# Performance work log

Measured on AMD Instinct MI355X. Metric: run time of the kernel, lower is better.

## Reference

```python
import jax, jax.numpy as jnp
from jax import lax
import numpy as np

H = 256      # encoder_hidden
F = 256      # variance predictor filter_size
K = 3        # kernel_size
NBINS = 256  # variance_embedding n_bins
B, S, T = 64, 512, 2048


def conv1d(x, w, b, pad):
    # x: [B, L, Cin], w: [K, Cin, Cout] -> [B, L, Cout]
    y = lax.conv_general_dilated(x, w, window_strides=(1,), padding=[(pad, pad)],
                                 dimension_numbers=('NWC', 'WIO', 'NWC'))
    return y + b


def layer_norm(x, g, b, eps=1e-5):
    mu = jnp.mean(x, -1, keepdims=True)
    v = jnp.mean((x - mu) ** 2, -1, keepdims=True)
    return (x - mu) * lax.rsqrt(v + eps) * g + b


def predictor(x, mask, w1, b1, g1, be1, w2, b2, g2, be2, lw, lb):
    h = jax.nn.relu(conv1d(x, w1, b1, (K - 1) // 2))
    h = layer_norm(h, g1, be1)
    h = jax.nn.relu(conv1d(h, w2, b2, 1))  # padding=1 hardcoded in original conv1d_2
    h = layer_norm(h, g2, be2)
    out = (h @ lw + lb)[..., 0]            # [B, L]
    return jnp.where(mask, 0.0, out)       # masked_fill(mask, 0.0)


def setup_inputs():
    key = jax.random.key(0)
    ks = jax.random.split(key, 16)
    inp = {
        'x': jax.random.normal(ks[0], (B, S, H), jnp.float32),
        'pitch_target': jax.random.normal(ks[1], (B, S), jnp.float32),
        'energy_target': jax.random.normal(ks[2], (B, S), jnp.float32),
        'src_mask': jnp.zeros((B, S), bool),
        'duration': jax.random.randint(ks[3], (B, S), 0, 4, jnp.int32),
        'max_len': T,
    }
    i = 4
    for p in ['d', 'p', 'e']:
        inp[p + '_w1'] = jax.random.normal(ks[i], (K, H, F), jnp.float32) * 0.05; i += 1
        inp[p + '_b1'] = jnp.zeros((F,), jnp.float32)
        inp[p + '_g1'] = jnp.ones((F,), jnp.float32)
        inp[p + '_be1'] = jnp.zeros((F,), jnp.float32)
        inp[p + '_w2'] = jax.random.normal(ks[i], (K, F, F), jnp.float32) * 0.05; i += 1
        inp[p + '_b2'] = jnp.zeros((F,), jnp.float32)
        inp[p + '_g2'] = jnp.ones((F,), jnp.float32)
        inp[p + '_be2'] = jnp.zeros((F,), jnp.float32)
        inp[p + '_lw'] = jax.random.normal(ks[i], (F, 1), jnp.float32) * 0.05; i += 1
        inp[p + '_lb'] = jnp.zeros((1,), jnp.float32)
    inp['p_table'] = jax.random.normal(ks[i], (NBINS, H), jnp.float32) * 0.02; i += 1
    inp['e_table'] = jax.random.normal(ks[i], (NBINS, H), jnp.float32) * 0.02
    return inp


def reference(x, pitch_target, energy_target, src_mask, duration, max_len,
              d_w1, d_b1, d_g1, d_be1, d_w2, d_b2, d_g2, d_be2, d_lw, d_lb,
              p_w1, p_b1, p_g1, p_be1, p_w2, p_b2, p_g2, p_be2, p_lw, p_lb,
              e_w1, e_b1, e_g1, e_be1, e_w2, e_b2, e_g2, e_be2, e_lw, e_lb,
              p_table, e_table):
    # linear-quantized bins over the data range (stats.json min/max -> [-2, 2] for randn data)
    bins = jnp.linspace(-2.0, 2.0, NBINS - 1, dtype=jnp.float32)

    log_d_pred = predictor(x, src_mask, d_w1, d_b1, d_g1, d_be1, d_w2, d_b2, d_g2, d_be2, d_lw, d_lb)

    # phoneme-level pitch (training path: target given -> embed bucketized target)
    p_pred = predictor(x, src_mask, p_w1, p_b1, p_g1, p_be1, p_w2, p_b2, p_g2, p_be2, p_lw, p_lb)
    p_emb = p_table[jnp.searchsorted(bins, pitch_target, side='left')]  # torch.bucketize(right=False)
    x = x + p_emb

    # phoneme-level energy (predictor runs on x AFTER pitch embedding, as in original)
    e_pred = predictor(x, src_mask, e_w1, e_b1, e_g1, e_be1, e_w2, e_b2, e_g2, e_be2, e_lw, e_lb)
    e_emb = e_table[jnp.searchsorted(bins, energy_target, side='left')]
    x = x + e_emb

    # Length regulation: expand phoneme i duration[b, i] times, pad to max_len.
    cum = jnp.cumsum(duration, axis=1)                 # [B, S]
    mel_len = cum[:, -1]                               # [B]
    frames = jnp.arange(max_len)                       # [T]
    # frame t maps to first phoneme i with cum[i] > t
    idx = jax.vmap(lambda c: jnp.searchsorted(c, frames, side='right'))(cum)  # [B, T]
    idx = jnp.minimum(idx, duration.shape[1] - 1)
    mel = jnp.take_along_axis(x, idx[:, :, None], axis=1)                     # [B, T, H]
    valid = frames[None, :] < mel_len[:, None]
    mel = jnp.where(valid[:, :, None], mel, 0.0)       # zero-pad beyond mel_len

    d_rounded = duration
    return (mel, p_pred, e_pred, log_d_pred, d_rounded, mel_len)
```

## Files before the change

kernel.cpp:

```cpp
#include <hip/hip_runtime.h>
#include <cstdint>
#include <cstddef>


#define HH 256
#define SS 512
#define BB 64
#define TT 2048
#define LSTR 264

typedef __bf16 bf16;
typedef __attribute__((ext_vector_type(8))) __bf16 bf16x8;
typedef __attribute__((ext_vector_type(4))) __bf16 bf16x4;
typedef __attribute__((ext_vector_type(4))) float f32x4;

static constexpr size_t WSZ = (size_t)3 * HH * HH;

__device__ __forceinline__ float edge_val(int j) {
    const float step = 4.0f / 254.0f;
    if (j == 254) return 2.0f;
    return __fadd_rn(-2.0f, __fmul_rn((float)j, step));
}
__device__ __forceinline__ int bucket256(float v) {
    int lo = 0, hi = 255;
    while (lo < hi) {
        int mid = (lo + hi) >> 1;
        if (edge_val(mid) < v) lo = mid + 1; else hi = mid;
    }
    return lo;
}

__global__ __launch_bounds__(256) void prep_kernel(
    const float* __restrict__ w0, const float* __restrict__ w1,
    const float* __restrict__ w2, const float* __restrict__ w3,
    const float* __restrict__ w4, const float* __restrict__ w5,
    bf16* __restrict__ wp,
    const int* __restrict__ dur, int* __restrict__ idxb, int* __restrict__ mli,
    float* __restrict__ drnd, float* __restrict__ mlen)
{
    const int tid = threadIdx.x;
    if (blockIdx.x < 18) {
        const int cv = blockIdx.x / 3, k = blockIdx.x % 3;
        const float* wsel[6] = {w0, w1, w2, w3, w4, w5};
        const float* wk = wsel[cv] + (size_t)k * HH * HH;
        bf16* o = wp + ((size_t)(cv * 3 + k)) * HH * HH;
        for (int fb = 0; fb < 16; ++fb) {
            #pragma unroll
            for (int h = 0; h < 2; ++h) {
                const int idx  = tid + 256 * h;
                const int kcb  = idx >> 6, lane = idx & 63;
                const int f    = fb * 16 + (lane & 15);
                const int c0   = kcb * 32 + (lane >> 4) * 8;
                bf16x8 v;
                #pragma unroll
                for (int j = 0; j < 8; ++j) v[j] = (bf16)wk[(size_t)(c0 + j) * HH + f];
                *(bf16x8*)(o + (((size_t)fb * 8 + kcb) * 64 + lane) * 8) = v;
            }
        }
    } else {
        __shared__ int sb[SS];
        const int b = blockIdx.x - 18;
        const int d0 = dur[b * SS + tid];
        const int d1 = dur[b * SS + tid + 256];
        drnd[b * SS + tid]       = (float)d0;
        drnd[b * SS + tid + 256] = (float)d1;
        sb[tid]       = d0;
        sb[tid + 256] = d1;
        __syncthreads();
        for (int off = 1; off < SS; off <<= 1) {
            const int a0 = (tid >= off) ? sb[tid - off] : 0;
            const int a1 = (tid + 256 >= off) ? sb[tid + 256 - off] : 0;
            __syncthreads();
            sb[tid] += a0;
            sb[tid + 256] += a1;
            __syncthreads();
        }
        {
            const int hi = sb[tid], lo = hi - d0;
            for (int j = lo; j < hi; ++j) idxb[b * TT + j] = tid;
        }
        {
            const int hi = sb[tid + 256], lo = hi - d1;
            for (int j = lo; j < hi; ++j) idxb[b * TT + j] = tid + 256;
        }
        if (tid == 255) { mlen[b] = (float)sb[SS - 1]; mli[b] = sb[SS - 1]; }
    }
}

struct Args3 {
    const float* bias[3];
    const float* g[3];
    const float* be[3];
    const float* lw[3];
    const float* lb[3];
    float*       out[3];
};

__global__ __launch_bounds__(256, 3) void conv_fused(
    const float* __restrict__ x,
    const float* __restrict__ pt,
    const float* __restrict__ ptab,
    const bf16* __restrict__ wpk,
    Args3 a1, Args3 a2,
    const uint8_t* __restrict__ mask)
{
    __shared__ alignas(16) bf16 tile[82 * LSTR];
    __shared__ float red_s[80][4], red_q[80][4];
    __shared__ float ln_m[80], ln_r[80];
    __shared__ int remb[82];

    const int tid    = threadIdx.x;
    const int pred   = blockIdx.x >> 9;
    const int within = blockIdx.x & 511;
    const int b      = within >> 3;
    const int s0     = (within & 7) * 64;
    const bool emb   = (pred == 2);

    const int lane = tid & 63;
    const int wv   = tid >> 6;

    const float* xb  = x + (size_t)b * SS * HH;
    const bf16* wt1 = wpk + (size_t)(pred * 2) * WSZ;
    const bf16* wt2 = wt1 + WSZ;

    if (emb) {
        if (tid < 82) {
            const int s = s0 - 9 + tid;
            remb[tid] = (s >= 0 && s < SS) ? bucket256(pt[b * SS + s]) : 0;
        }
        __syncthreads();
    }

    for (int idx = tid; idx < 82 * 64; idx += 256) {
        const int r  = idx >> 6, c4 = (idx & 63) << 2;
        const int s  = s0 - 9 + r;
        float4 v = make_float4(0.f, 0.f, 0.f, 0.f);
        if (s >= 0 && s < SS) {
            v = *(const float4*)(xb + (size_t)s * HH + c4);
            if (emb) {
                const float4 tv = *(const float4*)(ptab + (size_t)remb[r] * HH + c4);
                v.x += tv.x; v.y += tv.y; v.z += tv.z; v.w += tv.w;
            }
        }
        bf16x4 bv = {(bf16)v.x, (bf16)v.y, (bf16)v.z, (bf16)v.w};
        *(bf16x4*)&tile[r * LSTR + c4] = bv;
    }
    __syncthreads();

    const int ln15 = lane & 15;
    const int g8   = (lane >> 4) << 3;
    const int q4   = (lane >> 4) << 2;

    f32x4 bini[4];
    #pragma unroll
    for (int mf = 0; mf < 4; ++mf)
        #pragma unroll
        for (int i = 0; i < 4; ++i)
            bini[mf][i] = a1.bias[pred][64 * wv + 16 * mf + q4 + i];

    f32x4 acc1[4][5];
    #pragma unroll
    for (int mf = 0; mf < 4; ++mf)
        #pragma unroll
        for (int sf = 0; sf < 5; ++sf) acc1[mf][sf] = bini[mf];

    #pragma unroll 2
    for (int t = 0; t < 24; ++t) {
        const int k = t >> 3, kcb = t & 7;
        const int kc = kcb << 5;
        bf16x8 aw[4], bx[5];
        const bf16* bp = wt1 + ((((size_t)k * 16 + wv * 4) * 8 + kcb) << 9)
                       + (size_t)lane * 8;
        #pragma unroll
        for (int mf = 0; mf < 4; ++mf)
            aw[mf] = *(const bf16x8*)(bp + ((size_t)mf << 12));
        #pragma unroll
        for (int sf = 0; sf < 5; ++sf)
            bx[sf] = *(const bf16x8*)&tile[(16 * sf + ln15 + k) * LSTR + kc + g8];
        __builtin_amdgcn_s_setprio(1);
        #pragma unroll
        for (int mf = 0; mf < 4; ++mf)
            #pragma unroll
            for (int sf = 0; sf < 5; ++sf)
                acc1[mf][sf] = __builtin_amdgcn_mfma_f32_16x16x32_bf16(
                    aw[mf], bx[sf], acc1[mf][sf], 0, 0, 0);
        __builtin_amdgcn_s_setprio(0);
    }

    bf16x8 aw20[4];
    {
        const bf16* bp2 = wt2 + (((size_t)wv * 4) * 8 << 9) + (size_t)lane * 8;
        #pragma unroll
        for (int mf = 0; mf < 4; ++mf)
            aw20[mf] = *(const bf16x8*)(bp2 + ((size_t)mf << 12));
    }

    #pragma unroll
    for (int mf = 0; mf < 4; ++mf)
        #pragma unroll
        for (int sf = 0; sf < 5; ++sf)
            #pragma unroll
            for (int i = 0; i < 4; ++i)
                acc1[mf][sf][i] = fmaxf(acc1[mf][sf][i], 0.f);

    #pragma unroll
    for (int sf = 0; sf < 5; ++sf) {
        float s = 0.f, q = 0.f;
        #pragma unroll
        for (int mf = 0; mf < 4; ++mf)
            #pragma unroll
            for (int i = 0; i < 4; ++i) {
                const float v = acc1[mf][sf][i];
                s += v; q += v * v;
            }
        s += __shfl_xor(s, 16); s += __shfl_xor(s, 32);
        q += __shfl_xor(q, 16); q += __shfl_xor(q, 32);
        if (lane < 16) { red_s[16 * sf + lane][wv] = s; red_q[16 * sf + lane][wv] = q; }
    }
    __syncthreads();
    if (tid < 80) {
        const float s = red_s[tid][0] + red_s[tid][1] + red_s[tid][2] + red_s[tid][3];
        const float q = red_q[tid][0] + red_q[tid][1] + red_q[tid][2] + red_q[tid][3];
        const float mean = s * (1.f / 256.f);
        const float var  = q * (1.f / 256.f) - mean * mean;
        ln_m[tid] = mean;
        ln_r[tid] = rsqrtf(var + 1e-5f);
    }
    __syncthreads();

    {
        float g1v[4][4], be1v[4][4];
        #pragma unroll
        for (int mf = 0; mf < 4; ++mf)
            #pragma unroll
            for (int i = 0; i < 4; ++i) {
                const int f1 = 64 * wv + 16 * mf + q4 + i;
                g1v[mf][i]  = a1.g[pred][f1];
                be1v[mf][i] = a1.be[pred][f1];
            }
        #pragma unroll
        for (int sf = 0; sf < 5; ++sf) {
            const int o  = 16 * sf + ln15;
            const int hr = o - 7;
            const float mean = ln_m[o], rs = ln_r[o];
            const bool ok = (o >= 7 && o <= 72);
            #pragma unroll
            for (int mf = 0; mf < 4; ++mf) {
                bf16x4 hv;
                #pragma unroll
                for (int i = 0; i < 4; ++i)
                    hv[i] = (bf16)((acc1[mf][sf][i] - mean) * rs * g1v[mf][i] + be1v[mf][i]);
                if (ok)
                    *(bf16x4*)&tile[hr * LSTR + 64 * wv + 16 * mf + q4] = hv;
            }
        }
    }
    __syncthreads();
    if (tid < 64) {
        if (s0 == 0)       *(uint2*)&tile[tid * 4]            = make_uint2(0u, 0u);
        if (s0 == SS - 64) *(uint2*)&tile[65 * LSTR + tid * 4] = make_uint2(0u, 0u);
    }
    __syncthreads();

    #pragma unroll
    for (int mf = 0; mf < 4; ++mf)
        #pragma unroll
        for (int i = 0; i < 4; ++i)
            bini[mf][i] = a2.bias[pred][64 * wv + 16 * mf + q4 + i];

    f32x4 acc2[4][4];
    #pragma unroll
    for (int mf = 0; mf < 4; ++mf)
        #pragma unroll
        for (int sf = 0; sf < 4; ++sf) acc2[mf][sf] = bini[mf];

#define S2_STEP(AW_, K_, KCB_) do {                                            \
    const int kc_ = (KCB_) << 5;                                               \
    bf16x8 bx_[4];                                                             \
    _Pragma("unroll")                                                          \
    for (int sf_ = 0; sf_ < 4; ++sf_)                                          \
        bx_[sf_] = *(const bf16x8*)&tile[(16 * sf_ + ln15 + (K_)) * LSTR       \
                                         + kc_ + g8];                          \
    __builtin_amdgcn_s_setprio(1);                                             \
    _Pragma("unroll")                                                          \
    for (int mf_ = 0; mf_ < 4; ++mf_)                                          \
        _Pragma("unroll")                                                      \
        for (int sf_ = 0; sf_ < 4; ++sf_)                                      \
            acc2[mf_][sf_] = __builtin_amdgcn_mfma_f32_16x16x32_bf16(          \
                AW_[mf_], bx_[sf_], acc2[mf_][sf_], 0, 0, 0);                  \
    __builtin_amdgcn_s_setprio(0);                                             \
} while (0)

    S2_STEP(aw20, 0, 0);
    #pragma unroll 2
    for (int t = 1; t < 24; ++t) {
        const int k = t >> 3, kcb = t & 7;
        bf16x8 aw[4];
        const bf16* bp = wt2 + ((((size_t)k * 16 + wv * 4) * 8 + kcb) << 9)
                       + (size_t)lane * 8;
        #pragma unroll
        for (int mf = 0; mf < 4; ++mf)
            aw[mf] = *(const bf16x8*)(bp + ((size_t)mf << 12));
        S2_STEP(aw, k, kcb);
    }
#undef S2_STEP

    #pragma unroll
    for (int mf = 0; mf < 4; ++mf)
        #pragma unroll
        for (int sf = 0; sf < 4; ++sf)
            #pragma unroll
            for (int i = 0; i < 4; ++i)
                acc2[mf][sf][i] = fmaxf(acc2[mf][sf][i], 0.f);

    #pragma unroll
    for (int sf = 0; sf < 4; ++sf) {
        float s = 0.f, q = 0.f;
        #pragma unroll
        for (int mf = 0; mf < 4; ++mf)
            #pragma unroll
            for (int i = 0; i < 4; ++i) {
                const float v = acc2[mf][sf][i];
                s += v; q += v * v;
            }
        s += __shfl_xor(s, 16); s += __shfl_xor(s, 32);
        q += __shfl_xor(q, 16); q += __shfl_xor(q, 32);
        if (lane < 16) { red_s[16 * sf + lane][wv] = s; red_q[16 * sf + lane][wv] = q; }
    }
    __syncthreads();
    if (tid < 64) {
        const float s = red_s[tid][0] + red_s[tid][1] + red_s[tid][2] + red_s[tid][3];
        const float q = red_q[tid][0] + red_q[tid][1] + red_q[tid][2] + red_q[tid][3];
        const float mean = s * (1.f / 256.f);
        const float var  = q * (1.f / 256.f) - mean * mean;
        ln_m[tid] = mean;
        ln_r[tid] = rsqrtf(var + 1e-5f);
    }
    __syncthreads();

    {
        float c1v[4][4], cbv[4][4];
        #pragma unroll
        for (int mf = 0; mf < 4; ++mf)
            #pragma unroll
            for (int i = 0; i < 4; ++i) {
                const int f2 = 64 * wv + 16 * mf + q4 + i;
                const float lwv = a2.lw[pred][f2];
                c1v[mf][i] = a2.g[pred][f2] * lwv;
                cbv[mf][i] = a2.be[pred][f2] * lwv;
            }
        #pragma unroll
        for (int sf = 0; sf < 4; ++sf) {
            const int so = 16 * sf + ln15;
            const float mean = ln_m[so], rs = ln_r[so];
            float t = 0.f;
            #pragma unroll
            for (int mf = 0; mf < 4; ++mf)
                #pragma unroll
                for (int i = 0; i < 4; ++i)
                    t += (acc2[mf][sf][i] - mean) * rs * c1v[mf][i] + cbv[mf][i];
            t += __shfl_xor(t, 16); t += __shfl_xor(t, 32);
            if (lane < 16) red_s[16 * sf + lane][wv] = t;
        }
        __syncthreads();
        if (tid < 64) {
            const int gr = b * SS + s0 + tid;
            const float dv = red_s[tid][0] + red_s[tid][1] + red_s[tid][2] + red_s[tid][3]
                           + a2.lb[pred][0];
            a2.out[pred][gr] = mask[gr] ? 0.f : dv;
        }
    }
}

__global__ __launch_bounds__(256) void gather_kernel(
    const float* __restrict__ x,
    const float* __restrict__ ptab, const float* __restrict__ pt,
    const float* __restrict__ etab, const float* __restrict__ et,
    const int* __restrict__ idxb, const int* __restrict__ mli,
    float* __restrict__ mel)
{
    const int lane = threadIdx.x & 63;
    for (int row = blockIdx.x * 4 + (threadIdx.x >> 6); row < BB * TT; row += 4096 * 4) {
        const int b = row >> 11;
        const int t = row & (TT - 1);
        float4 v = make_float4(0.f, 0.f, 0.f, 0.f);
        if (t < mli[b]) {
            const int idx = idxb[row];
            const size_t src = ((size_t)b * SS + idx) * HH + lane * 4;
            v = *(const float4*)(x + src);
            const int pb = bucket256(pt[b * SS + idx]);
            const int eb = bucket256(et[b * SS + idx]);
            const float4 pv = *(const float4*)(ptab + (size_t)pb * HH + lane * 4);
            const float4 ev = *(const float4*)(etab + (size_t)eb * HH + lane * 4);
            v.x += pv.x + ev.x; v.y += pv.y + ev.y; v.z += pv.z + ev.z; v.w += pv.w + ev.w;
        }
        *(float4*)(mel + (size_t)row * HH + lane * 4) = v;
    }
}

extern "C" void kernel_launch(void* const* d_in, const int* in_sizes, int n_in,
                              void* d_out, int out_size, void* d_ws, size_t ws_size,
                              hipStream_t stream) {
    (void)in_sizes; (void)n_in; (void)out_size; (void)ws_size;

    const float*   x      = (const float*)d_in[0];
    const float*   pitch  = (const float*)d_in[1];
    const float*   energy = (const float*)d_in[2];
    const uint8_t* mask   = (const uint8_t*)d_in[3];
    const int*     dur    = (const int*)d_in[4];
    const float*   ptab   = (const float*)d_in[36];
    const float*   etab   = (const float*)d_in[37];

    float* out = (float*)d_out;
    const size_t N_MEL = (size_t)BB * TT * HH;
    float* out_p  = out + N_MEL;
    float* out_e  = out_p + (size_t)BB * SS;
    float* out_ld = out_e + (size_t)BB * SS;
    float* out_dr = out_ld + (size_t)BB * SS;
    float* out_ml = out_dr + (size_t)BB * SS;

    bf16* wpk  = (bf16*)d_ws;
    int*  idxb = (int*)(wpk + 6 * WSZ);
    int*  mli  = idxb + (size_t)BB * TT;

    prep_kernel<<<18 + 64, 256, 0, stream>>>(
        (const float*)d_in[6],  (const float*)d_in[10],
        (const float*)d_in[16], (const float*)d_in[20],
        (const float*)d_in[26], (const float*)d_in[30],
        wpk,
        dur, idxb, mli, out_dr, out_ml);

    Args3 a1 = {
        {(const float*)d_in[7],  (const float*)d_in[17], (const float*)d_in[27]},
        {(const float*)d_in[8],  (const float*)d_in[18], (const float*)d_in[28]},
        {(const float*)d_in[9],  (const float*)d_in[19], (const float*)d_in[29]},
        {nullptr, nullptr, nullptr}, {nullptr, nullptr, nullptr},
        {nullptr, nullptr, nullptr}
    };
    Args3 a2 = {
        {(const float*)d_in[11], (const float*)d_in[21], (const float*)d_in[31]},
        {(const float*)d_in[12], (const float*)d_in[22], (const float*)d_in[32]},
        {(const float*)d_in[13], (const float*)d_in[23], (const float*)d_in[33]},
        {(const float*)d_in[14], (const float*)d_in[24], (const float*)d_in[34]},
        {(const float*)d_in[15], (const float*)d_in[25], (const float*)d_in[35]},
        {out_ld, out_p, out_e}
    };

    conv_fused<<<3 * 512, 256, 0, stream>>>(x, pitch, ptab, wpk, a1, a2, mask);

    gather_kernel<<<4096, 256, 0, stream>>>(x, ptab, pitch, etab, energy, idxb, mli, out);
}
```

Before: 132.4 us.

## Run all three predictors in one block reusing a shared x tile

Instead of launching one block per (predictor, sequence tile), each block now loads the x tile once into shared memory and loops over the three predictors. The pitch embedding is added in place to the bf16 tile before the energy predictor. The conv1 output goes to a separate htile, which also holds the reduction scratch. This cuts the number of x loads and conversions by three, but leaves only 512 blocks with lower occupancy (launch bounds 2), so each block's serial work triples and latency is less well hidden. The embedding add also rounds to bf16 once more than the old fp32 add did.

```diff
diff --git a/kernel.cpp b/kernel.cpp
--- a/kernel.cpp
+++ b/kernel.cpp
@@ -96,7 +96,7 @@
     float*       out[3];
 };
 
-__global__ __launch_bounds__(256, 3) void conv_fused(
+__global__ __launch_bounds__(256, 2) void conv_all3(
     const float* __restrict__ x,
     const float* __restrict__ pt,
     const float* __restrict__ ptab,
@@ -104,46 +104,31 @@
     Args3 a1, Args3 a2,
     const uint8_t* __restrict__ mask)
 {
-    __shared__ alignas(16) bf16 tile[82 * LSTR];
-    __shared__ float red_s[80][4], red_q[80][4];
+    __shared__ alignas(16) bf16 xtile[82 * LSTR];
+    __shared__ alignas(16) bf16 htile[66 * LSTR];
     __shared__ float ln_m[80], ln_r[80];
     __shared__ int remb[82];
-
-    const int tid    = threadIdx.x;
-    const int pred   = blockIdx.x >> 9;
-    const int within = blockIdx.x & 511;
-    const int b      = within >> 3;
-    const int s0     = (within & 7) * 64;
-    const bool emb   = (pred == 2);
-
+    float* red = (float*)htile;
+
+    const int tid  = threadIdx.x;
+    const int b    = blockIdx.x >> 3;
+    const int s0   = (blockIdx.x & 7) * 64;
     const int lane = tid & 63;
     const int wv   = tid >> 6;
 
-    const float* xb  = x + (size_t)b * SS * HH;
-    const bf16* wt1 = wpk + (size_t)(pred * 2) * WSZ;
-    const bf16* wt2 = wt1 + WSZ;
-
-    if (emb) {
-        if (tid < 82) {
-            const int s = s0 - 9 + tid;
-            remb[tid] = (s >= 0 && s < SS) ? bucket256(pt[b * SS + s]) : 0;
-        }
-        __syncthreads();
-    }
-
+    const float* xb = x + (size_t)b * SS * HH;
+
+    if (tid < 82) {
+        const int s = s0 - 9 + tid;
+        remb[tid] = (s >= 0 && s < SS) ? bucket256(pt[b * SS + s]) : 0;
+    }
     for (int idx = tid; idx < 82 * 64; idx += 256) {
-        const int r  = idx >> 6, c4 = (idx & 63) << 2;
-        const int s  = s0 - 9 + r;
+        const int r = idx >> 6, c4 = (idx & 63) << 2;
+        const int s = s0 - 9 + r;
         float4 v = make_float4(0.f, 0.f, 0.f, 0.f);
-        if (s >= 0 && s < SS) {
-            v = *(const float4*)(xb + (size_t)s * HH + c4);
-            if (emb) {
-                const float4 tv = *(const float4*)(ptab + (size_t)remb[r] * HH + c4);
-                v.x += tv.x; v.y += tv.y; v.z += tv.z; v.w += tv.w;
-            }
-        }
+        if (s >= 0 && s < SS) v = *(const float4*)(xb + (size_t)s * HH + c4);
         bf16x4 bv = {(bf16)v.x, (bf16)v.y, (bf16)v.z, (bf16)v.w};
-        *(bf16x4*)&tile[r * LSTR + c4] = bv;
+        *(bf16x4*)&xtile[r * LSTR + c4] = bv;
     }
     __syncthreads();
 
@@ -151,136 +136,159 @@
     const int g8   = (lane >> 4) << 3;
     const int q4   = (lane >> 4) << 2;
 
-    f32x4 bini[4];
-    #pragma unroll
-    for (int mf = 0; mf < 4; ++mf)
-        #pragma unroll
-        for (int i = 0; i < 4; ++i)
-            bini[mf][i] = a1.bias[pred][64 * wv + 16 * mf + q4 + i];
-
-    f32x4 acc1[4][5];
-    #pragma unroll
-    for (int mf = 0; mf < 4; ++mf)
-        #pragma unroll
-        for (int sf = 0; sf < 5; ++sf) acc1[mf][sf] = bini[mf];
-
-    #pragma unroll 2
-    for (int t = 0; t < 24; ++t) {
-        const int k = t >> 3, kcb = t & 7;
-        const int kc = kcb << 5;
-        bf16x8 aw[4], bx[5];
-        const bf16* bp = wt1 + ((((size_t)k * 16 + wv * 4) * 8 + kcb) << 9)
-                       + (size_t)lane * 8;
-        #pragma unroll
-        for (int mf = 0; mf < 4; ++mf)
-            aw[mf] = *(const bf16x8*)(bp + ((size_t)mf << 12));
-        #pragma unroll
-        for (int sf = 0; sf < 5; ++sf)
-            bx[sf] = *(const bf16x8*)&tile[(16 * sf + ln15 + k) * LSTR + kc + g8];
-        __builtin_amdgcn_s_setprio(1);
-        #pragma unroll
-        for (int mf = 0; mf < 4; ++mf)
+    #pragma unroll 1
+    for (int pred = 0; pred < 3; ++pred) {
+        if (pred == 2) {
+            for (int idx = tid; idx < 82 * 64; idx += 256) {
+                const int r = idx >> 6, c4 = (idx & 63) << 2;
+                bf16x4 v = *(bf16x4*)&xtile[r * LSTR + c4];
+                const float4 tv = *(const float4*)(ptab + (size_t)remb[r] * HH + c4);
+                v[0] = (bf16)((float)v[0] + tv.x);
+                v[1] = (bf16)((float)v[1] + tv.y);
+                v[2] = (bf16)((float)v[2] + tv.z);
+                v[3] = (bf16)((float)v[3] + tv.w);
+                *(bf16x4*)&xtile[r * LSTR + c4] = v;
+            }
+            __syncthreads();
+        }
+
+        const bf16* wt1 = wpk + (size_t)(pred * 2) * WSZ;
+        const bf16* wt2 = wt1 + WSZ;
+
+        f32x4 bini[4];
+        #pragma unroll
+        for (int mf = 0; mf < 4; ++mf)
+            #pragma unroll
+            for (int i = 0; i < 4; ++i)
+                bini[mf][i] = a1.bias[pred][64 * wv + 16 * mf + q4 + i];
+
+        f32x4 acc1[4][5];
+        #pragma unroll
+        for (int mf = 0; mf < 4; ++mf)
+            #pragma unroll
+            for (int sf = 0; sf < 5; ++sf) acc1[mf][sf] = bini[mf];
+
+        #pragma unroll 2
+        for (int t = 0; t < 24; ++t) {
+            const int k = t >> 3, kcb = t & 7;
+            const int kc = kcb << 5;
+            bf16x8 aw[4], bx[5];
+            const bf16* bp = wt1 + ((((size_t)k * 16 + wv * 4) * 8 + kcb) << 9)
+                           + (size_t)lane * 8;
+            #pragma unroll
+            for (int mf = 0; mf < 4; ++mf)
+                aw[mf] = *(const bf16x8*)(bp + ((size_t)mf << 12));
             #pragma unroll
             for (int sf = 0; sf < 5; ++sf)
-                acc1[mf][sf] = __builtin_amdgcn_mfma_f32_16x16x32_bf16(
-                    aw[mf], bx[sf], acc1[mf][sf], 0, 0, 0);
-        __builtin_amdgcn_s_setprio(0);
-    }
-
-    bf16x8 aw20[4];
-    {
-        const bf16* bp2 = wt2 + (((size_t)wv * 4) * 8 << 9) + (size_t)lane * 8;
-        #pragma unroll
-        for (int mf = 0; mf < 4; ++mf)
-            aw20[mf] = *(const bf16x8*)(bp2 + ((size_t)mf << 12));
-    }
-
-    #pragma unroll
-    for (int mf = 0; mf < 4; ++mf)
-        #pragma unroll
-        for (int sf = 0; sf < 5; ++sf)
+                bx[sf] = *(const bf16x8*)&xtile[(16 * sf + ln15 + k) * LSTR + kc + g8];
+            __builtin_amdgcn_s_setprio(1);
+            #pragma unroll
+            for (int mf = 0; mf < 4; ++mf)
+                #pragma unroll
+                for (int sf = 0; sf < 5; ++sf)
+                    acc1[mf][sf] = __builtin_amdgcn_mfma_f32_16x16x32_bf16(
+                        aw[mf], bx[sf], acc1[mf][sf], 0, 0, 0);
+            __builtin_amdgcn_s_setprio(0);
+        }
+
+        bf16x8 aw20[4];
+        {
+            const bf16* bp2 = wt2 + (((size_t)wv * 4) * 8 << 9) + (size_t)lane * 8;
+            #pragma unroll
+            for (int mf = 0; mf < 4; ++mf)
+                aw20[mf] = *(const bf16x8*)(bp2 + ((size_t)mf << 12));
+        }
+
+        #pragma unroll
+        for (int mf = 0; mf < 4; ++mf)
+            #pragma unroll
+            for (int sf = 0; sf < 5; ++sf)
+                #pragma unroll
+                for (int i = 0; i < 4; ++i)
+                    acc1[mf][sf][i] = fmaxf(acc1[mf][sf][i], 0.f);
+
+        #pragma unroll
+        for (int sf = 0; sf < 5; ++sf) {
+            float s = 0.f, q = 0.f;
+            #pragma unroll
+            for (int mf = 0; mf < 4; ++mf)
+                #pragma unroll
+                for (int i = 0; i < 4; ++i) {
+                    const float v = acc1[mf][sf][i];
+                    s += v; q += v * v;
+                }
+            s += __shfl_xor(s, 16); s += __shfl_xor(s, 32);
+            q += __shfl_xor(q, 16); q += __shfl_xor(q, 32);
+            if (lane < 16) {
+                red[(16 * sf + lane) * 4 + wv] = s;
+                red[320 + (16 * sf + lane) * 4 + wv] = q;
+            }
+        }
+        __syncthreads();
+        if (tid < 80) {
+            const float s = red[tid * 4] + red[tid * 4 + 1] + red[tid * 4 + 2] + red[tid * 4 + 3];
+            const float q = red[320 + tid * 4] + red[320 + tid * 4 + 1]
+                          + red[320 + tid * 4 + 2] + red[320 + tid * 4 + 3];
+            const float mean = s * (1.f / 256.f);
+            const float var  = q * (1.f / 256.f) - mean * mean;
+            ln_m[tid] = mean;
+            ln_r[tid] = rsqrtf(var + 1e-5f);
+        }
+        __syncthreads();
+
+        {
+            float g1v[4][4], be1v[4][4];
+            #pragma unroll
+            for (int mf = 0; mf < 4; ++mf)
+                #pragma unroll
+                for (int i = 0; i < 4; ++i) {
+                    const int f1 = 64 * wv + 16 * mf + q4 + i;
+                    g1v[mf][i]  = a1.g[pred][f1];
+                    be1v[mf][i] = a1.be[pred][f1];
+                }
+            #pragma unroll
+            for (int sf = 0; sf < 5; ++sf) {
+                const int o  = 16 * sf + ln15;
+                const int hr = o - 7;
+                const float mean = ln_m[o], rs = ln_r[o];
+                const bool ok = (o >= 7 && o <= 72);
+                #pragma unroll
+                for (int mf = 0; mf < 4; ++mf) {
+                    bf16x4 hv;
+                    #pragma unroll
+                    for (int i = 0; i < 4; ++i)
+                        hv[i] = (bf16)((acc1[mf][sf][i] - mean) * rs * g1v[mf][i] + be1v[mf][i]);
+                    if (ok)
+                        *(bf16x4*)&htile[hr * LSTR + 64 * wv + 16 * mf + q4] = hv;
+                }
+            }
+        }
+        __syncthreads();
+        if (tid < 64) {
+            if (s0 == 0)       *(uint2*)&htile[tid * 4]            = make_uint2(0u, 0u);
+            if (s0 == SS - 64) *(uint2*)&htile[65 * LSTR + tid * 4] = make_uint2(0u, 0u);
+        }
+        __syncthreads();
+
+        #pragma unroll
+        for (int mf = 0; mf < 4; ++mf)
             #pragma unroll
             for (int i = 0; i < 4; ++i)
-                acc1[mf][sf][i] = fmaxf(acc1[mf][sf][i], 0.f);
-
-    #pragma unroll
-    for (int sf = 0; sf < 5; ++sf) {
-        float s = 0.f, q = 0.f;
-        #pragma unroll
-        for (int mf = 0; mf < 4; ++mf)
-            #pragma unroll
-            for (int i = 0; i < 4; ++i) {
-                const float v = acc1[mf][sf][i];
-                s += v; q += v * v;
-            }
-        s += __shfl_xor(s, 16); s += __shfl_xor(s, 32);
-        q += __shfl_xor(q, 16); q += __shfl_xor(q, 32);
-        if (lane < 16) { red_s[16 * sf + lane][wv] = s; red_q[16 * sf + lane][wv] = q; }
-    }
-    __syncthreads();
-    if (tid < 80) {
-        const float s = red_s[tid][0] + red_s[tid][1] + red_s[tid][2] + red_s[tid][3];
-        const float q = red_q[tid][0] + red_q[tid][1] + red_q[tid][2] + red_q[tid][3];
-        const float mean = s * (1.f / 256.f);
-        const float var  = q * (1.f / 256.f) - mean * mean;
-        ln_m[tid] = mean;
-        ln_r[tid] = rsqrtf(var + 1e-5f);
-    }
-    __syncthreads();
-
-    {
-        float g1v[4][4], be1v[4][4];
-        #pragma unroll
-        for (int mf = 0; mf < 4; ++mf)
-            #pragma unroll
-            for (int i = 0; i < 4; ++i) {
-                const int f1 = 64 * wv + 16 * mf + q4 + i;
-                g1v[mf][i]  = a1.g[pred][f1];
-                be1v[mf][i] = a1.be[pred][f1];
-            }
-        #pragma unroll
-        for (int sf = 0; sf < 5; ++sf) {
-            const int o  = 16 * sf + ln15;
-            const int hr = o - 7;
-            const float mean = ln_m[o], rs = ln_r[o];
-            const bool ok = (o >= 7 && o <= 72);
-            #pragma unroll
-            for (int mf = 0; mf < 4; ++mf) {
-                bf16x4 hv;
-                #pragma unroll
-                for (int i = 0; i < 4; ++i)
-                    hv[i] = (bf16)((acc1[mf][sf][i] - mean) * rs * g1v[mf][i] + be1v[mf][i]);
-                if (ok)
-                    *(bf16x4*)&tile[hr * LSTR + 64 * wv + 16 * mf + q4] = hv;
-            }
-        }
-    }
-    __syncthreads();
-    if (tid < 64) {
-        if (s0 == 0)       *(uint2*)&tile[tid * 4]            = make_uint2(0u, 0u);
-        if (s0 == SS - 64) *(uint2*)&tile[65 * LSTR + tid * 4] = make_uint2(0u, 0u);
-    }
-    __syncthreads();
-
-    #pragma unroll
-    for (int mf = 0; mf < 4; ++mf)
-        #pragma unroll
-        for (int i = 0; i < 4; ++i)
-            bini[mf][i] = a2.bias[pred][64 * wv + 16 * mf + q4 + i];
-
-    f32x4 acc2[4][4];
-    #pragma unroll
-    for (int mf = 0; mf < 4; ++mf)
-        #pragma unroll
-        for (int sf = 0; sf < 4; ++sf) acc2[mf][sf] = bini[mf];
+                bini[mf][i] = a2.bias[pred][64 * wv + 16 * mf + q4 + i];
+
+        f32x4 acc2[4][4];
+        #pragma unroll
+        for (int mf = 0; mf < 4; ++mf)
+            #pragma unroll
+            for (int sf = 0; sf < 4; ++sf) acc2[mf][sf] = bini[mf];
 
 #define S2_STEP(AW_, K_, KCB_) do {                                            \
     const int kc_ = (KCB_) << 5;                                               \
     bf16x8 bx_[4];                                                             \
     _Pragma("unroll")                                                          \
     for (int sf_ = 0; sf_ < 4; ++sf_)                                          \
-        bx_[sf_] = *(const bf16x8*)&tile[(16 * sf_ + ln15 + (K_)) * LSTR       \
-                                         + kc_ + g8];                          \
+        bx_[sf_] = *(const bf16x8*)&htile[(16 * sf_ + ln15 + (K_)) * LSTR      \
+                                          + kc_ + g8];                         \
     __builtin_amdgcn_s_setprio(1);                                             \
     _Pragma("unroll")                                                          \
     for (int mf_ = 0; mf_ < 4; ++mf_)                                          \
@@ -291,84 +299,92 @@
     __builtin_amdgcn_s_setprio(0);                                             \
 } while (0)
 
-    S2_STEP(aw20, 0, 0);
-    #pragma unroll 2
-    for (int t = 1; t < 24; ++t) {
-        const int k = t >> 3, kcb = t & 7;
-        bf16x8 aw[4];
-        const bf16* bp = wt2 + ((((size_t)k * 16 + wv * 4) * 8 + kcb) << 9)
-                       + (size_t)lane * 8;
-        #pragma unroll
-        for (int mf = 0; mf < 4; ++mf)
-            aw[mf] = *(const bf16x8*)(bp + ((size_t)mf << 12));
-        S2_STEP(aw, k, kcb);
-    }
+        S2_STEP(aw20, 0, 0);
+        #pragma unroll 2
+        for (int t = 1; t < 24; ++t) {
+            const int k = t >> 3, kcb = t & 7;
+            bf16x8 aw[4];
+            const bf16* bp = wt2 + ((((size_t)k * 16 + wv * 4) * 8 + kcb) << 9)
+                           + (size_t)lane * 8;
+            #pragma unroll
+            for (int mf = 0; mf < 4; ++mf)
+                aw[mf] = *(const bf16x8*)(bp + ((size_t)mf << 12));
+            S2_STEP(aw, k, kcb);
+        }
 #undef S2_STEP
 
-    #pragma unroll
-    for (int mf = 0; mf < 4; ++mf)
-        #pragma unroll
-        for (int sf = 0; sf < 4; ++sf)
-            #pragma unroll
-            for (int i = 0; i < 4; ++i)
-                acc2[mf][sf][i] = fmaxf(acc2[mf][sf][i], 0.f);
-
-    #pragma unroll
-    for (int sf = 0; sf < 4; ++sf) {
-        float s = 0.f, q = 0.f;
-        #pragma unroll
-        for (int mf = 0; mf < 4; ++mf)
-            #pragma unroll
-            for (int i = 0; i < 4; ++i) {
-                const float v = acc2[mf][sf][i];
-                s += v; q += v * v;
-            }
-        s += __shfl_xor(s, 16); s += __shfl_xor(s, 32);
-        q += __shfl_xor(q, 16); q += __shfl_xor(q, 32);
-        if (lane < 16) { red_s[16 * sf + lane][wv] = s; red_q[16 * sf + lane][wv] = q; }
-    }
-    __syncthreads();
-    if (tid < 64) {
-        const float s = red_s[tid][0] + red_s[tid][1] + red_s[tid][2] + red_s[tid][3];
-        const float q = red_q[tid][0] + red_q[tid][1] + red_q[tid][2] + red_q[tid][3];
-        const float mean = s * (1.f / 256.f);
-        const float var  = q * (1.f / 256.f) - mean * mean;
-        ln_m[tid] = mean;
-        ln_r[tid] = rsqrtf(var + 1e-5f);
-    }
-    __syncthreads();
-
-    {
-        float c1v[4][4], cbv[4][4];
-        #pragma unroll
-        for (int mf = 0; mf < 4; ++mf)
-            #pragma unroll
-            for (int i = 0; i < 4; ++i) {
-                const int f2 = 64 * wv + 16 * mf + q4 + i;
-                const float lwv = a2.lw[pred][f2];
-                c1v[mf][i] = a2.g[pred][f2] * lwv;
-                cbv[mf][i] = a2.be[pred][f2] * lwv;
-            }
+        #pragma unroll
+        for (int mf = 0; mf < 4; ++mf)
+            #pragma unroll
+            for (int sf = 0; sf < 4; ++sf)
+                #pragma unroll
+                for (int i = 0; i < 4; ++i)
+                    acc2[mf][sf][i] = fmaxf(acc2[mf][sf][i], 0.f);
+
+        __syncthreads();
+
         #pragma unroll
         for (int sf = 0; sf < 4; ++sf) {
-            const int so = 16 * sf + ln15;
-            const float mean = ln_m[so], rs = ln_r[so];
-            float t = 0.f;
-            #pragma unroll
-            for (int mf = 0; mf < 4; ++mf)
-                #pragma unroll
-                for (int i = 0; i < 4; ++i)
-                    t += (acc2[mf][sf][i] - mean) * rs * c1v[mf][i] + cbv[mf][i];
-            t += __shfl_xor(t, 16); t += __shfl_xor(t, 32);
-            if (lane < 16) red_s[16 * sf + lane][wv] = t;
+            float s = 0.f, q = 0.f;
+            #pragma unroll
+            for (int mf = 0; mf < 4; ++mf)
+                #pragma unroll
+                for (int i = 0; i < 4; ++i) {
+                    const float v = acc2[mf][sf][i];
+                    s += v; q += v * v;
+                }
+            s += __shfl_xor(s, 16); s += __shfl_xor(s, 32);
+            q += __shfl_xor(q, 16); q += __shfl_xor(q, 32);
+            if (lane < 16) {
+                red[(16 * sf + lane) * 4 + wv] = s;
+                red[320 + (16 * sf + lane) * 4 + wv] = q;
+            }
         }
         __syncthreads();
         if (tid < 64) {
-            const int gr = b * SS + s0 + tid;
-            const float dv = red_s[tid][0] + red_s[tid][1] + red_s[tid][2] + red_s[tid][3]
-                           + a2.lb[pred][0];
-            a2.out[pred][gr] = mask[gr] ? 0.f : dv;
-        }
+            const float s = red[tid * 4] + red[tid * 4 + 1] + red[tid * 4 + 2] + red[tid * 4 + 3];
+            const float q = red[320 + tid * 4] + red[320 + tid * 4 + 1]
+                          + red[320 + tid * 4 + 2] + red[320 + tid * 4 + 3];
+            const float mean = s * (1.f / 256.f);
+            const float var  = q * (1.f / 256.f) - mean * mean;
+            ln_m[tid] = mean;
+            ln_r[tid] = rsqrtf(var + 1e-5f);
+        }
+        __syncthreads();
+
+        {
+            float c1v[4][4], cbv[4][4];
+            #pragma unroll
+            for (int mf = 0; mf < 4; ++mf)
+                #pragma unroll
+                for (int i = 0; i < 4; ++i) {
+                    const int f2 = 64 * wv + 16 * mf + q4 + i;
+                    const float lwv = a2.lw[pred][f2];
+                    c1v[mf][i] = a2.g[pred][f2] * lwv;
+                    cbv[mf][i] = a2.be[pred][f2] * lwv;
+                }
+            #pragma unroll
+            for (int sf = 0; sf < 4; ++sf) {
+                const int so = 16 * sf + ln15;
+                const float mean = ln_m[so], rs = ln_r[so];
+                float t = 0.f;
+                #pragma unroll
+                for (int mf = 0; mf < 4; ++mf)
+                    #pragma unroll
+                    for (int i = 0; i < 4; ++i)
+                        t += (acc2[mf][sf][i] - mean) * rs * c1v[mf][i] + cbv[mf][i];
+                t += __shfl_xor(t, 16); t += __shfl_xor(t, 32);
+                if (lane < 16) red[(16 * sf + lane) * 4 + wv] = t;
+            }
+            __syncthreads();
+            if (tid < 64) {
+                const int gr = b * SS + s0 + tid;
+                const float dv = red[tid * 4] + red[tid * 4 + 1] + red[tid * 4 + 2]
+                               + red[tid * 4 + 3] + a2.lb[pred][0];
+                a2.out[pred][gr] = mask[gr] ? 0.f : dv;
+            }
+        }
+        __syncthreads();
     }
 }
 
@@ -446,7 +462,7 @@
         {out_ld, out_p, out_e}
     };
 
-    conv_fused<<<3 * 512, 256, 0, stream>>>(x, pitch, ptab, wpk, a1, a2, mask);
+    conv_all3<<<512, 256, 0, stream>>>(x, pitch, ptab, wpk, a1, a2, mask);
 
     gather_kernel<<<4096, 256, 0, stream>>>(x, ptab, pitch, etab, energy, idxb, mli, out);
 }
```

Measured after the change: 138.1 us. 1.04x slower.
